# Kernel optimization log

Measured on AMD Instinct MI355X. Metric: run time of the kernel, lower is better.

## Reference

```python
import jax, jax.numpy as jnp
import numpy as np

N_NODES = 30000; SEQ_LEN = 32; VOCAB = 10000
RNN_H = 128; RGCN_IN = 64; RGCN_H = 64; N_CLASSES = 16
N_RELS = 8; N_BASES = 4; N_EDGES = 480000


def setup_inputs() -> dict:
    key = jax.random.key(0)
    ks = jax.random.split(key, 20)
    s = 0.05
    norm = lambda k, shape: jax.random.normal(k, shape, jnp.float32) * s
    return {
        "inputs": jax.random.randint(ks[0], (N_NODES, SEQ_LEN), 0, VOCAB),
        "sequence_length": jax.random.randint(ks[1], (N_NODES,), 1, SEQ_LEN),
        "src": jax.random.randint(ks[2], (N_EDGES,), 0, N_NODES),
        "dst": jax.random.randint(ks[3], (N_EDGES,), 0, N_NODES),
        "rel_type": jax.random.randint(ks[4], (N_EDGES,), 0, N_RELS),
        "edge_norm": jax.random.uniform(ks[5], (N_EDGES,), jnp.float32),
        # RNN encoder params (only reverse-direction LSTM affects the output h_n[-1])
        "emb": norm(ks[6], (VOCAB, RNN_H)),
        "w_ih": norm(ks[7], (4 * RNN_H, RNN_H)),
        "w_hh": norm(ks[8], (4 * RNN_H, RNN_H)),
        "b_ih": norm(ks[9], (4 * RNN_H,)),
        "b_hh": norm(ks[10], (4 * RNN_H,)),
        "fc_w": norm(ks[11], (RGCN_IN, RNN_H)),
        "fc_b": norm(ks[12], (RGCN_IN,)),
        # RGCN basis-decomposed weights: W_r = sum_b w_comp[r,b] * basis[b]
        "basis0": norm(ks[13], (N_BASES, RGCN_IN, RGCN_H)),
        "wcomp0": norm(ks[14], (N_RELS, N_BASES)),
        "basis1": norm(ks[15], (N_BASES, RGCN_H, RGCN_H)),
        "wcomp1": norm(ks[16], (N_RELS, N_BASES)),
        "basis2": norm(ks[17], (N_BASES, RGCN_H, N_CLASSES)),
        "wcomp2": norm(ks[18], (N_RELS, N_BASES)),
    }


def _lstm_last(x, w_ih, w_hh, b_ih, b_hh):
    # x: [T, B, H] -> final hidden state [B, H] (PyTorch gate order: i, f, g, o)
    H = w_hh.shape[1]
    B = x.shape[1]
    h0 = jnp.zeros((B, H), x.dtype)

    def step(carry, x_t):
        h, c = carry
        z = x_t @ w_ih.T + b_ih + h @ w_hh.T + b_hh
        i, f, g, o = jnp.split(z, 4, axis=-1)
        c = jax.nn.sigmoid(f) * c + jax.nn.sigmoid(i) * jnp.tanh(g)
        h = jax.nn.sigmoid(o) * jnp.tanh(c)
        return (h, c), None

    (h, _), _ = jax.lax.scan(step, (h0, h0), x)
    return h


def _rgcn_layer(h, src, dst, rel, norm, basis, w_comp, activation):
    # Basis-decomposed RGCN: aggregate normed source feats per (dst, rel), then transform.
    # Mathematically identical to per-edge h[src] @ W[rel] scatter-summed to dst.
    n = h.shape[0]
    R = w_comp.shape[0]
    W = jnp.einsum('rb,bio->rio', w_comp, basis)            # [R, in, out]
    msg = h[src] * norm[:, None]                            # [E, in] gather
    seg = dst * R + rel                                     # scatter key (dst, rel)
    agg = jax.ops.segment_sum(msg, seg, num_segments=n * R)
    agg = agg.reshape(n, R, -1)                             # [N, R, in]
    out = jnp.einsum('nri,rio->no', agg, W)                 # [N, out]
    return activation(out) if activation is not None else out


def reference(inputs, sequence_length, src, dst, rel_type, edge_norm,
              emb, w_ih, w_hh, b_ih, b_hh, fc_w, fc_b,
              basis0, wcomp0, basis1, wcomp1, basis2, wcomp2):
    # RNN encoder: embedding -> bidirectional LSTM -> fc(h_n[-1]).
    # h_n[-1] is the reverse-direction final state, so only the reverse LSTM
    # pass affects the output; run it on the time-reversed sequence.
    x = emb[inputs.T]                                       # [T, N, H]
    h_last = _lstm_last(x[::-1], w_ih, w_hh, b_ih, b_hh)    # [N, H]
    feats = h_last @ fc_w.T + fc_b                          # [N, RGCN_IN]
    # RGCN: input/hidden layers with relu, output layer without activation.
    h = _rgcn_layer(feats, src, dst, rel_type, edge_norm, basis0, wcomp0, jax.nn.relu)
    h = _rgcn_layer(h, src, dst, rel_type, edge_norm, basis1, wcomp1, jax.nn.relu)
    h = _rgcn_layer(h, src, dst, rel_type, edge_norm, basis2, wcomp2, None)
    return h
```

## Files before the change

kernel.cpp:

```cpp
#include <hip/hip_runtime.h>

typedef float  f32x4  __attribute__((ext_vector_type(4)));
typedef short  bf16x8 __attribute__((ext_vector_type(8)));
typedef unsigned int   u32;
typedef unsigned short u16;

#define N_NODES 30000
#define VOCABSZ 10000
#define LOG2E 1.442695040888963f

__device__ __forceinline__ float sigm(float x){
  return __builtin_amdgcn_rcpf(1.f + __builtin_amdgcn_exp2f(-LOG2E*x));
}
__device__ __forceinline__ float tanh_(float x){
  return 1.f - 2.f*__builtin_amdgcn_rcpf(1.f + __builtin_amdgcn_exp2f((2.f*LOG2E)*x));
}
__device__ __forceinline__ u16 f2bf(float f){
  u32 u = __builtin_bit_cast(u32, f);
  u = u + 0x7fffu + ((u>>16)&1u);
  return (u16)(u>>16);
}
__device__ __forceinline__ float bflo(u32 u){ return __builtin_bit_cast(float, u<<16); }
__device__ __forceinline__ float bfhi(u32 u){ return __builtin_bit_cast(float, u & 0xffff0000u); }

__global__ __launch_bounds__(256) void wmat_kernel(
    const float* __restrict__ b0, const float* __restrict__ c0,
    const float* __restrict__ b1, const float* __restrict__ c1,
    const float* __restrict__ b2, const float* __restrict__ c2,
    float* __restrict__ W0, float* __restrict__ W1, float* __restrict__ W2)
{
  int id = blockIdx.x*256 + threadIdx.x;
  if (id < 32768){
    int r = id>>12;
    float s = 0.f;
    #pragma unroll
    for (int b=0;b<4;++b) s += c0[r*4+b]*b0[b*4096 + (id&4095)];
    W0[id] = s;
  } else if (id < 65536){
    int k = id - 32768;
    int r = k>>12;
    float s = 0.f;
    #pragma unroll
    for (int b=0;b<4;++b) s += c1[r*4+b]*b1[b*4096 + (k&4095)];
    W1[k] = s;
  } else if (id < 73728){
    int k = id - 65536;
    int r = k>>10;
    float s = 0.f;
    #pragma unroll
    for (int b=0;b<4;++b) s += c2[r*4+b]*b2[b*1024 + (k&1023)];
    W2[k] = s;
  }
}

__global__ __launch_bounds__(256) void embproj_kernel(
    const float* __restrict__ emb, const float* __restrict__ w_ih,
    const float* __restrict__ b_ih, const float* __restrict__ b_hh,
    u16* __restrict__ eproj)
{
  __shared__ float et[64*132];
  __shared__ float wt[32*132];
  const int tid = threadIdx.x;
  const int v0 = blockIdx.x*64;
  const int vq = tid>>4, jq = tid&15;

  for (int idx = tid*4; idx < 64*128; idx += 1024){
    int row = idx>>7, col = idx&127;
    int vr = v0 + row; if (vr > VOCABSZ-1) vr = VOCABSZ-1;
    *(f32x4*)&et[row*132+col] = *(const f32x4*)&emb[vr*128+col];
  }
  for (int jt=0; jt<16; ++jt){
    __syncthreads();
    for (int idx = tid*4; idx < 32*128; idx += 1024){
      int row = idx>>7, col = idx&127;
      *(f32x4*)&wt[row*132+col] = *(const f32x4*)&w_ih[(jt*32+row)*128+col];
    }
    __syncthreads();
    float acc[4][2] = {};
    #pragma unroll 4
    for (int k=0;k<128;++k){
      float w0v = wt[(jq*2+0)*132+k];
      float w1v = wt[(jq*2+1)*132+k];
      #pragma unroll
      for (int a=0;a<4;++a){
        float e = et[(vq*4+a)*132+k];
        acc[a][0] += e*w0v;
        acc[a][1] += e*w1v;
      }
    }
    int jb = jt*32 + jq*2;
    float bi0 = b_ih[jb]   + b_hh[jb];
    float bi1 = b_ih[jb+1] + b_hh[jb+1];
    int g  = jb>>7, rem = jb&127;
    int w  = rem>>4, q4 = (rem>>2)&3, jl = rem&3;
    int jp = w*64 + q4*16 + jl*4 + g;
    #pragma unroll
    for (int a=0;a<4;++a){
      int v = v0 + vq*4 + a;
      if (v < VOCABSZ){
        eproj[v*512 + jp]     = f2bf(acc[a][0]+bi0);
        eproj[v*512 + jp + 4] = f2bf(acc[a][1]+bi1);
      }
    }
  }
}

__global__ __launch_bounds__(512, 2) void lstm_kernel(
    const int* __restrict__ tok, const u16* __restrict__ eproj,
    const float* __restrict__ w_hh, const float* __restrict__ fc_w,
    const float* __restrict__ fc_b, float* __restrict__ feats)
{
  __shared__ __align__(16) char lds[65536];
  __shared__ int tokL[128*33];
  const int tid = threadIdx.x;
  const int wave = tid>>6, lane = tid&63;
  const int c16 = lane&15, g4 = lane>>4;
  const int nb = blockIdx.x*128;

  bf16x8 afr[4][4];
  #pragma unroll
  for (int g=0; g<4; ++g){
    const float* wr = w_hh + (g*128 + wave*16 + c16)*128 + g4*8;
    #pragma unroll
    for (int kk=0; kk<4; ++kk){
      f32x4 wa = *(const f32x4*)(wr + kk*32);
      f32x4 wbv = *(const f32x4*)(wr + kk*32 + 4);
      bf16x8 a;
      a[0]=(short)f2bf(wa[0]); a[1]=(short)f2bf(wa[1]);
      a[2]=(short)f2bf(wa[2]); a[3]=(short)f2bf(wa[3]);
      a[4]=(short)f2bf(wbv[0]); a[5]=(short)f2bf(wbv[1]);
      a[6]=(short)f2bf(wbv[2]); a[7]=(short)f2bf(wbv[3]);
      afr[g][kk] = a;
    }
  }
  {
    f32x4 z = {0.f,0.f,0.f,0.f};
    for (int i = tid*16; i < 32768; i += 8192) *(f32x4*)(lds + i) = z;
  }
  {
    int n = tid>>2, t0 = (tid&3)*8;
    int node = nb + n; if (node > N_NODES-1) node = N_NODES-1;
    int4 a = *(const int4*)(tok + node*32 + t0);
    int4 b = *(const int4*)(tok + node*32 + t0 + 4);
    int* dstp = &tokL[n*33 + t0];
    dstp[0]=a.x; dstp[1]=a.y; dstp[2]=a.z; dstp[3]=a.w;
    dstp[4]=b.x; dstp[5]=b.y; dstp[6]=b.z; dstp[7]=b.w;
  }
  const int swz = (c16&7)<<4;
  int rb[4];
  #pragma unroll
  for (int kk=0;kk<4;++kk) rb[kk] = c16*256 + ((kk*64 + g4*16)^swz);
  const int wbB = c16*256 + ((wave*32 + g4*8)^swz);

  float creg[8][4];
  #pragma unroll
  for (int nt=0;nt<8;++nt)
    #pragma unroll
    for (int q=0;q<4;++q) creg[nt][q]=0.f;

  __syncthreads();

  const size_t gbase = (size_t)(wave*128 + g4*32);
  uint4 gxX[8], gxY[8];
  #pragma unroll
  for (int nt=0;nt<8;++nt){
    int ptok = tokL[(nt*16+c16)*33 + 31];
    const char* ep = (const char*)eproj + (size_t)ptok*1024 + gbase;
    gxX[nt] = *(const uint4*)ep;
    gxY[nt] = *(const uint4*)(ep+16);
  }

  for (int t=0; t<32; ++t){
    const int bufR = (t&1)<<15, bufW = bufR ^ 32768;
    int ptk[8];
    if (t < 31){
      #pragma unroll
      for (int nt=0;nt<8;++nt) ptk[nt] = tokL[(nt*16+c16)*33 + 30 - t];
    }
    #pragma unroll
    for (int nt=0; nt<8; ++nt){
      uint4 X = gxX[nt], Y = gxY[nt];
      f32x4 acc[4];
      acc[0][0]=bflo(X.x); acc[1][0]=bfhi(X.x); acc[2][0]=bflo(X.y); acc[3][0]=bfhi(X.y);
      acc[0][1]=bflo(X.z); acc[1][1]=bfhi(X.z); acc[2][1]=bflo(X.w); acc[3][1]=bfhi(X.w);
      acc[0][2]=bflo(Y.x); acc[1][2]=bfhi(Y.x); acc[2][2]=bflo(Y.y); acc[3][2]=bfhi(Y.y);
      acc[0][3]=bflo(Y.z); acc[1][3]=bfhi(Y.z); acc[2][3]=bflo(Y.w); acc[3][3]=bfhi(Y.w);
      if (t < 31){
        const char* ep = (const char*)eproj + (size_t)ptk[nt]*1024 + gbase;
        gxX[nt] = *(const uint4*)ep;
        gxY[nt] = *(const uint4*)(ep+16);
      }
      bf16x8 bfr[4];
      #pragma unroll
      for (int kk=0;kk<4;++kk)
        bfr[kk] = *(const bf16x8*)(lds + bufR + rb[kk] + nt*4096);
      #pragma unroll
      for (int kk=0;kk<4;++kk){
        acc[0] = __builtin_amdgcn_mfma_f32_16x16x32_bf16(afr[0][kk], bfr[kk], acc[0], 0,0,0);
        acc[1] = __builtin_amdgcn_mfma_f32_16x16x32_bf16(afr[1][kk], bfr[kk], acc[1], 0,0,0);
        acc[2] = __builtin_amdgcn_mfma_f32_16x16x32_bf16(afr[2][kk], bfr[kk], acc[2], 0,0,0);
        acc[3] = __builtin_amdgcn_mfma_f32_16x16x32_bf16(afr[3][kk], bfr[kk], acc[3], 0,0,0);
      }
      float hv[4];
      #pragma unroll
      for (int q=0;q<4;++q){
        float zi=acc[0][q], zf=acc[1][q], zg=acc[2][q], zo=acc[3][q];
        float cn = sigm(zf)*creg[nt][q] + sigm(zi)*tanh_(zg);
        creg[nt][q] = cn;
        hv[q] = sigm(zo)*tanh_(cn);
      }
      u32 plo, phi;
      asm("v_cvt_pk_bf16_f32 %0, %1, %2" : "=v"(plo) : "v"(hv[0]), "v"(hv[1]));
      asm("v_cvt_pk_bf16_f32 %0, %1, %2" : "=v"(phi) : "v"(hv[2]), "v"(hv[3]));
      uint2 hw; hw.x = plo; hw.y = phi;
      *(uint2*)(lds + bufW + wbB + nt*4096) = hw;
    }
    __syncthreads();
  }
  f32x4 fca[4];
  #pragma unroll
  for (int ot=0;ot<4;++ot){ fca[ot][0]=0.f; fca[ot][1]=0.f; fca[ot][2]=0.f; fca[ot][3]=0.f; }
  #pragma unroll
  for (int kk=0;kk<4;++kk){
    bf16x8 b = *(const bf16x8*)(lds + rb[kk] + wave*4096);
    #pragma unroll
    for (int ot=0;ot<4;++ot){
      const float* fr = fc_w + (ot*16 + c16)*128 + kk*32 + g4*8;
      f32x4 wa = *(const f32x4*)fr;
      f32x4 wbv = *(const f32x4*)(fr+4);
      bf16x8 a;
      a[0]=(short)f2bf(wa[0]); a[1]=(short)f2bf(wa[1]);
      a[2]=(short)f2bf(wa[2]); a[3]=(short)f2bf(wa[3]);
      a[4]=(short)f2bf(wbv[0]); a[5]=(short)f2bf(wbv[1]);
      a[6]=(short)f2bf(wbv[2]); a[7]=(short)f2bf(wbv[3]);
      fca[ot] = __builtin_amdgcn_mfma_f32_16x16x32_bf16(a, b, fca[ot], 0,0,0);
    }
  }
  const int node = nb + wave*16 + c16;
  if (node < N_NODES){
    #pragma unroll
    for (int ot=0;ot<4;++ot)
      #pragma unroll
      for (int q=0;q<4;++q){
        int o = ot*16 + g4*4 + q;
        feats[node*64 + o] = fca[ot][q] + fc_b[o];
      }
  }
}

template<int NO, bool RELU>
__global__ __launch_bounds__(256) void transform_kernel(
    const float* __restrict__ h, const float* __restrict__ W,
    float* __restrict__ tmp, int n_nodes)
{
  __shared__ float As[64][68];
  __shared__ float Bs[64][132];
  const int tid = threadIdx.x;
  const int n0 = blockIdx.x*64;
  const int j0 = blockIdx.y*128;
  constexpr int WIDTH = 8*NO;

  for (int idx = tid*4; idx < 4096; idx += 1024){
    int r = idx>>6, c = idx&63;
    int n = n0 + r; if (n > n_nodes-1) n = n_nodes-1;
    f32x4 v = *(const f32x4*)(h + (size_t)n*64 + c);
    if (RELU){
      v[0]=fmaxf(v[0],0.f); v[1]=fmaxf(v[1],0.f);
      v[2]=fmaxf(v[2],0.f); v[3]=fmaxf(v[3],0.f);
    }
    *(f32x4*)&As[r][c] = v;
  }
  for (int idx = tid*4; idx < 8192; idx += 1024){
    int k = idx>>7, j = idx&127;
    int jj = j0 + j;
    int r = jj / NO, o = jj & (NO-1);
    f32x4 v = *(const f32x4*)(W + r*(64*NO) + k*NO + o);
    *(f32x4*)&Bs[k][j] = v;
  }
  __syncthreads();

  const int tx = tid&15, ty = tid>>4;
  float acc[4][8];
  #pragma unroll
  for (int i=0;i<4;++i)
    #pragma unroll
    for (int j=0;j<8;++j) acc[i][j]=0.f;

  #pragma unroll 4
  for (int k=0;k<64;++k){
    f32x4 b0 = *(const f32x4*)&Bs[k][tx*8];
    f32x4 b1 = *(const f32x4*)&Bs[k][tx*8+4];
    #pragma unroll
    for (int i=0;i<4;++i){
      float a = As[ty*4+i][k];
      #pragma unroll
      for (int j=0;j<4;++j){
        acc[i][j]   += a*b0[j];
        acc[i][j+4] += a*b1[j];
      }
    }
  }
  #pragma unroll
  for (int i=0;i<4;++i){
    int n = n0 + ty*4 + i;
    if (n < n_nodes){
      *(f32x4*)(tmp + (size_t)n*WIDTH + j0 + tx*8)     = *(f32x4*)&acc[i][0];
      *(f32x4*)(tmp + (size_t)n*WIDTH + j0 + tx*8 + 4) = *(f32x4*)&acc[i][4];
    }
  }
}

template<int NO>
__global__ __launch_bounds__(256) void scatter_kernel(
    const float* __restrict__ tmp, const int* __restrict__ src,
    const int* __restrict__ dst, const int* __restrict__ rel,
    const float* __restrict__ enorm, float* __restrict__ out, int n_edges)
{
  constexpr int EPW = 64/NO;
  constexpr int WIDTH = 8*NO;
  const int lane = threadIdx.x & 63;
  const int es = (NO==64) ? 0 : (lane>>4);
  const int o  = lane & (NO-1);
  const long gw = (long)((blockIdx.x*256 + threadIdx.x)>>6);
  const long stride = (long)gridDim.x*4*EPW;
  long e = gw*EPW + es;
  if (e >= n_edges) return;
  int s=src[e], d=dst[e], r=rel[e]; float nm=enorm[e];
  float v = tmp[(size_t)s*WIDTH + r*NO + o];
  while (true){
    long e1 = e + stride;
    bool more = (e1 < n_edges);
    int s1=0,d1=0,r1=0; float nm1=0.f, v1=0.f;
    if (more){
      s1=src[e1]; d1=dst[e1]; r1=rel[e1]; nm1=enorm[e1];
      v1 = tmp[(size_t)s1*WIDTH + r1*NO + o];
    }
    unsafeAtomicAdd(out + (size_t)d*NO + o, v*nm);
    if (!more) break;
    s=s1; d=d1; r=r1; nm=nm1; v=v1; e=e1;
  }
}

extern "C" void kernel_launch(void* const* d_in, const int* in_sizes, int n_in,
                              void* d_out, int out_size, void* d_ws, size_t ws_size,
                              hipStream_t stream)
{
  const int*   tok    = (const int*)  d_in[0];
  const int*   src    = (const int*)  d_in[2];
  const int*   dst    = (const int*)  d_in[3];
  const int*   rel    = (const int*)  d_in[4];
  const float* enorm  = (const float*)d_in[5];
  const float* emb    = (const float*)d_in[6];
  const float* w_ih   = (const float*)d_in[7];
  const float* w_hh   = (const float*)d_in[8];
  const float* b_ih   = (const float*)d_in[9];
  const float* b_hh   = (const float*)d_in[10];
  const float* fc_w   = (const float*)d_in[11];
  const float* fc_b   = (const float*)d_in[12];
  const float* basis0 = (const float*)d_in[13];
  const float* wcomp0 = (const float*)d_in[14];
  const float* basis1 = (const float*)d_in[15];
  const float* wcomp1 = (const float*)d_in[16];
  const float* basis2 = (const float*)d_in[17];
  const float* wcomp2 = (const float*)d_in[18];

  char* ws = (char*)d_ws;
  float* tmp   = (float*)(ws);
  u16*   eproj = (u16*)  (ws);
  float* feats = (float*)(ws + 61440000);
  float* g1    = (float*)(ws + 69120000);
  float* g2    = (float*)(ws + 76800000);
  float* W0    = (float*)(ws + 84480000);
  float* W1    = (float*)(ws + 84611072);
  float* W2    = (float*)(ws + 84742144);

  wmat_kernel<<<288, 256, 0, stream>>>(basis0, wcomp0, basis1, wcomp1,
                                       basis2, wcomp2, W0, W1, W2);
  embproj_kernel<<<157, 256, 0, stream>>>(emb, w_ih, b_ih, b_hh, eproj);
  lstm_kernel<<<235, 512, 0, stream>>>(tok, eproj, w_hh, fc_w, fc_b, feats);

  transform_kernel<64,false><<<dim3(469,4), 256, 0, stream>>>(feats, W0, tmp, N_NODES);
  hipMemsetAsync(g1, 0, 30000*64*4, stream);
  scatter_kernel<64><<<2048, 256, 0, stream>>>(tmp, src, dst, rel, enorm, g1, 480000);

  transform_kernel<64,true><<<dim3(469,4), 256, 0, stream>>>(g1, W1, tmp, N_NODES);
  hipMemsetAsync(g2, 0, 30000*64*4, stream);
  scatter_kernel<64><<<2048, 256, 0, stream>>>(tmp, src, dst, rel, enorm, g2, 480000);

  transform_kernel<16,true><<<dim3(469,1), 256, 0, stream>>>(g2, W2, tmp, N_NODES);
  hipMemsetAsync(d_out, 0, 30000*16*4, stream);
  scatter_kernel<16><<<2048, 256, 0, stream>>>(tmp, src, dst, rel, enorm, (float*)d_out, 480000);
}
```

Measured before the change: 736.3 us.

## Halve LSTM node tile per block, split embproj over gate tiles, batch memsets

The LSTM kernel now handles 64 nodes per 512-thread block instead of 128, giving 469 blocks instead of 235. It shrinks LDS use (u16 token cache, half-size hidden buffers) and register state so more of the GPU's compute units stay busy, at the cost of loading the w_hh fragments twice as often. The embedding-projection kernel is split across a second grid dimension of 4 gate-tile groups for more parallelism. The three separate memsets are collapsed into two launched early, with g1 and g2 zeroed by one contiguous call.

```diff
diff --git a/kernel.cpp b/kernel.cpp
--- a/kernel.cpp
+++ b/kernel.cpp
@@ -69,7 +69,7 @@
     int vr = v0 + row; if (vr > VOCABSZ-1) vr = VOCABSZ-1;
     *(f32x4*)&et[row*132+col] = *(const f32x4*)&emb[vr*128+col];
   }
-  for (int jt=0; jt<16; ++jt){
+  for (int jt = blockIdx.y*4; jt < blockIdx.y*4 + 4; ++jt){
     __syncthreads();
     for (int idx = tid*4; idx < 32*128; idx += 1024){
       int row = idx>>7, col = idx&127;
@@ -110,12 +110,12 @@
     const float* __restrict__ w_hh, const float* __restrict__ fc_w,
     const float* __restrict__ fc_b, float* __restrict__ feats)
 {
-  __shared__ __align__(16) char lds[65536];
-  __shared__ int tokL[128*33];
+  __shared__ __align__(16) char lds[32768];
+  __shared__ u16 tokL[64*33];
   const int tid = threadIdx.x;
   const int wave = tid>>6, lane = tid&63;
   const int c16 = lane&15, g4 = lane>>4;
-  const int nb = blockIdx.x*128;
+  const int nb = blockIdx.x*64;
 
   bf16x8 afr[4][4];
   #pragma unroll
@@ -135,16 +135,16 @@
   }
   {
     f32x4 z = {0.f,0.f,0.f,0.f};
-    for (int i = tid*16; i < 32768; i += 8192) *(f32x4*)(lds + i) = z;
+    for (int i = tid*16; i < 16384; i += 8192) *(f32x4*)(lds + i) = z;
   }
   {
-    int n = tid>>2, t0 = (tid&3)*8;
+    int n = tid>>3, t0 = (tid&7)*4;
     int node = nb + n; if (node > N_NODES-1) node = N_NODES-1;
     int4 a = *(const int4*)(tok + node*32 + t0);
-    int4 b = *(const int4*)(tok + node*32 + t0 + 4);
-    int* dstp = &tokL[n*33 + t0];
-    dstp[0]=a.x; dstp[1]=a.y; dstp[2]=a.z; dstp[3]=a.w;
-    dstp[4]=b.x; dstp[5]=b.y; dstp[6]=b.z; dstp[7]=b.w;
+    tokL[n*33 + t0    ] = (u16)a.x;
+    tokL[n*33 + t0 + 1] = (u16)a.y;
+    tokL[n*33 + t0 + 2] = (u16)a.z;
+    tokL[n*33 + t0 + 3] = (u16)a.w;
   }
   const int swz = (c16&7)<<4;
   int rb[4];
@@ -152,18 +152,18 @@
   for (int kk=0;kk<4;++kk) rb[kk] = c16*256 + ((kk*64 + g4*16)^swz);
   const int wbB = c16*256 + ((wave*32 + g4*8)^swz);
 
-  float creg[8][4];
-  #pragma unroll
-  for (int nt=0;nt<8;++nt)
+  float creg[4][4];
+  #pragma unroll
+  for (int nt=0;nt<4;++nt)
     #pragma unroll
     for (int q=0;q<4;++q) creg[nt][q]=0.f;
 
   __syncthreads();
 
   const size_t gbase = (size_t)(wave*128 + g4*32);
-  uint4 gxX[8], gxY[8];
-  #pragma unroll
-  for (int nt=0;nt<8;++nt){
+  uint4 gxX[4], gxY[4];
+  #pragma unroll
+  for (int nt=0;nt<4;++nt){
     int ptok = tokL[(nt*16+c16)*33 + 31];
     const char* ep = (const char*)eproj + (size_t)ptok*1024 + gbase;
     gxX[nt] = *(const uint4*)ep;
@@ -171,14 +171,14 @@
   }
 
   for (int t=0; t<32; ++t){
-    const int bufR = (t&1)<<15, bufW = bufR ^ 32768;
-    int ptk[8];
+    const int bufR = (t&1)<<14, bufW = bufR ^ 16384;
+    int ptk[4];
     if (t < 31){
       #pragma unroll
-      for (int nt=0;nt<8;++nt) ptk[nt] = tokL[(nt*16+c16)*33 + 30 - t];
-    }
-    #pragma unroll
-    for (int nt=0; nt<8; ++nt){
+      for (int nt=0;nt<4;++nt) ptk[nt] = tokL[(nt*16+c16)*33 + 30 - t];
+    }
+    #pragma unroll
+    for (int nt=0; nt<4; ++nt){
       uint4 X = gxX[nt], Y = gxY[nt];
       f32x4 acc[4];
       acc[0][0]=bflo(X.x); acc[1][0]=bfhi(X.x); acc[2][0]=bflo(X.y); acc[3][0]=bfhi(X.y);
@@ -217,14 +217,16 @@
     }
     __syncthreads();
   }
-  f32x4 fca[4];
-  #pragma unroll
-  for (int ot=0;ot<4;++ot){ fca[ot][0]=0.f; fca[ot][1]=0.f; fca[ot][2]=0.f; fca[ot][3]=0.f; }
+  const int w2 = wave>>1, half = wave&1;
+  f32x4 fca[2];
+  #pragma unroll
+  for (int oi=0;oi<2;++oi){ fca[oi][0]=0.f; fca[oi][1]=0.f; fca[oi][2]=0.f; fca[oi][3]=0.f; }
   #pragma unroll
   for (int kk=0;kk<4;++kk){
-    bf16x8 b = *(const bf16x8*)(lds + rb[kk] + wave*4096);
-    #pragma unroll
-    for (int ot=0;ot<4;++ot){
+    bf16x8 b = *(const bf16x8*)(lds + rb[kk] + w2*4096);
+    #pragma unroll
+    for (int oi=0;oi<2;++oi){
+      int ot = half*2 + oi;
       const float* fr = fc_w + (ot*16 + c16)*128 + kk*32 + g4*8;
       f32x4 wa = *(const f32x4*)fr;
       f32x4 wbv = *(const f32x4*)(fr+4);
@@ -233,17 +235,17 @@
       a[2]=(short)f2bf(wa[2]); a[3]=(short)f2bf(wa[3]);
       a[4]=(short)f2bf(wbv[0]); a[5]=(short)f2bf(wbv[1]);
       a[6]=(short)f2bf(wbv[2]); a[7]=(short)f2bf(wbv[3]);
-      fca[ot] = __builtin_amdgcn_mfma_f32_16x16x32_bf16(a, b, fca[ot], 0,0,0);
-    }
-  }
-  const int node = nb + wave*16 + c16;
+      fca[oi] = __builtin_amdgcn_mfma_f32_16x16x32_bf16(a, b, fca[oi], 0,0,0);
+    }
+  }
+  const int node = nb + w2*16 + c16;
   if (node < N_NODES){
     #pragma unroll
-    for (int ot=0;ot<4;++ot)
+    for (int oi=0;oi<2;++oi)
       #pragma unroll
       for (int q=0;q<4;++q){
-        int o = ot*16 + g4*4 + q;
-        feats[node*64 + o] = fca[ot][q] + fc_b[o];
+        int o = (half*2+oi)*16 + g4*4 + q;
+        feats[node*64 + o] = fca[oi][q] + fc_b[o];
       }
   }
 }
@@ -376,18 +378,19 @@
 
   wmat_kernel<<<288, 256, 0, stream>>>(basis0, wcomp0, basis1, wcomp1,
                                        basis2, wcomp2, W0, W1, W2);
-  embproj_kernel<<<157, 256, 0, stream>>>(emb, w_ih, b_ih, b_hh, eproj);
-  lstm_kernel<<<235, 512, 0, stream>>>(tok, eproj, w_hh, fc_w, fc_b, feats);
+  embproj_kernel<<<dim3(157,4), 256, 0, stream>>>(emb, w_ih, b_ih, b_hh, eproj);
+
+  hipMemsetAsync(g1, 0, 15360000, stream);
+  hipMemsetAsync(d_out, 0, 30000*16*4, stream);
+
+  lstm_kernel<<<469, 512, 0, stream>>>(tok, eproj, w_hh, fc_w, fc_b, feats);
 
   transform_kernel<64,false><<<dim3(469,4), 256, 0, stream>>>(feats, W0, tmp, N_NODES);
-  hipMemsetAsync(g1, 0, 30000*64*4, stream);
   scatter_kernel<64><<<2048, 256, 0, stream>>>(tmp, src, dst, rel, enorm, g1, 480000);
 
   transform_kernel<64,true><<<dim3(469,4), 256, 0, stream>>>(g1, W1, tmp, N_NODES);
-  hipMemsetAsync(g2, 0, 30000*64*4, stream);
   scatter_kernel<64><<<2048, 256, 0, stream>>>(tmp, src, dst, rel, enorm, g2, 480000);
 
   transform_kernel<16,true><<<dim3(469,1), 256, 0, stream>>>(g2, W2, tmp, N_NODES);
-  hipMemsetAsync(d_out, 0, 30000*16*4, stream);
   scatter_kernel<16><<<2048, 256, 0, stream>>>(tmp, src, dst, rel, enorm, (float*)d_out, 480000);
 }
```

Result: faster. 685.4 us (-6.9%).
